# Kernel optimization log

Hardware: AMD Instinct MI355X
Metric: run time of the kernel (lower is better)

Reference implementation:

```python
import jax, jax.numpy as jnp
import numpy as np

K = 10
BN_EPS = 1e-5


def _edgeconv(x, W, b, gamma, beta):
    """DGCNN EdgeConv: kNN on x, edge feat [x_i, x_j - x_i], Linear->(BN)->ReLU, max over k.
    x: [N, C]; W: [2C, Cout]; gamma/beta: [Cout] or None."""
    sq = jnp.sum(x * x, axis=1)                      # [N]
    dist = sq[:, None] + sq[None, :] - 2.0 * (x @ x.T)  # [N, N] squared dists
    _, idx = jax.lax.top_k(-dist, K)                 # [N, K] (includes self)
    xj = x[idx]                                      # [N, K, C] gather
    xi = jnp.broadcast_to(x[:, None, :], xj.shape)   # [N, K, C]
    e = jnp.concatenate([xi, xj - xi], axis=-1)      # [N, K, 2C]
    h = e @ W + b                                    # [N, K, Cout]
    if gamma is not None:                            # BatchNorm1d (training-mode batch stats)
        mu = h.mean(axis=(0, 1))
        var = h.var(axis=(0, 1))
        h = (h - mu) * jax.lax.rsqrt(var + BN_EPS) * gamma + beta
    h = jax.nn.relu(h)
    return h.max(axis=1)                             # [N, Cout]


def _aggregate(f, seg_ids, num_segments):
    return jax.ops.segment_max(f, seg_ids, num_segments=num_segments)


def setup_inputs() -> dict:
    key = jax.random.key(0)
    ks = jax.random.split(key, 12)
    N, B = 16384, 64
    x = jax.random.normal(ks[0], (N, 3), dtype=jnp.float32)
    n_pts = jnp.full((B,), N // B, dtype=jnp.int32)

    def lin(k, fi, fo):
        s = 1.0 / np.sqrt(fi)
        kw, kb = jax.random.split(k)
        return (jax.random.uniform(kw, (fi, fo), jnp.float32, -s, s),
                jax.random.uniform(kb, (fo,), jnp.float32, -s, s))

    W1, b1 = lin(ks[1], 6, 64)
    W2, b2 = lin(ks[2], 128, 64)
    W3, b3 = lin(ks[3], 128, 64)
    W4, b4 = lin(ks[4], 128, 64)
    Wp, bp = lin(ks[5], 256, 128)
    g1 = jnp.ones((64,), jnp.float32); be1 = jnp.zeros((64,), jnp.float32)
    g3 = jnp.ones((64,), jnp.float32); be3 = jnp.zeros((64,), jnp.float32)
    return {"x": x, "n_pts": n_pts,
            "W1": W1, "b1": b1, "g1": g1, "be1": be1,
            "W2": W2, "b2": b2,
            "W3": W3, "b3": b3, "g3": g3, "be3": be3,
            "W4": W4, "b4": b4,
            "Wp": Wp, "bp": bp}


def reference(x, n_pts, W1, b1, g1, be1, W2, b2, W3, b3, g3, be3, W4, b4, Wp, bp):
    N = x.shape[0]
    B = n_pts.shape[0]
    seg_ids = jnp.repeat(jnp.arange(B, dtype=jnp.int32), n_pts, total_repeat_length=N)

    f1 = _edgeconv(x,  W1, b1, g1,  be1)   # [N, 64]
    f2 = _edgeconv(f1, W2, b2, None, None)
    f3 = _edgeconv(f2, W3, b3, g3,  be3)
    f4 = _edgeconv(f3, W4, b4, None, None)

    p = jnp.concatenate([_aggregate(f, seg_ids, B) for f in (f1, f2, f3, f4)], axis=1)  # [B, 256]
    f = jnp.tanh(p @ Wp + bp)              # [B, 128]
    f = f / (jnp.linalg.norm(f, axis=1, keepdims=True) + 1e-9)
    return f
```

## Files before the change

kernel.cpp:

```cpp
#include <hip/hip_runtime.h>
#include <hip/hip_bf16.h>

constexpr int N = 16384;
constexpr int KNN = 10;
constexpr int CF = 64;
constexpr int NS64 = 12;
constexpr int NS3 = 6;

#define FBIG 1e30f

typedef __attribute__((ext_vector_type(8))) __bf16 bfv8;
typedef __attribute__((ext_vector_type(4))) float f32x4;

#define TOPK_INSERT(dval, jval)                                            \
  if ((dval) < bmax) {                                                     \
    float mv = bd[0]; int slot = 0;                                        \
    _Pragma("unroll") for (int s_ = 1; s_ < 10; ++s_)                      \
      if (bd[s_] > mv) { mv = bd[s_]; slot = s_; }                         \
    _Pragma("unroll") for (int s_ = 0; s_ < 10; ++s_)                      \
      if (slot == s_) { bd[s_] = (dval); bi[s_] = (jval); }                \
    bmax = bd[0];                                                          \
    _Pragma("unroll") for (int s_ = 1; s_ < 10; ++s_)                      \
      bmax = fmaxf(bmax, bd[s_]);                                          \
  }

__device__ inline ushort bf16_rne(float x) {
  unsigned u = __float_as_uint(x);
  return (ushort)((u + 0x7FFFu + ((u >> 16) & 1u)) >> 16);
}
__device__ inline float bf16_to_f(ushort h) { return __uint_as_float(((unsigned)h) << 16); }

__global__ __launch_bounds__(256) void pack3_kernel(const float* __restrict__ X,
                                                    float4* __restrict__ xp) {
  int i = blockIdx.x * 256 + threadIdx.x;
  float x0 = X[3 * i], x1 = X[3 * i + 1], x2 = X[3 * i + 2];
  float s = fmaf(x0, x0, fmaf(x1, x1, x2 * x2));
  xp[i] = make_float4(x0, x1, x2, s);
}

__global__ __launch_bounds__(256) void prep128s_kernel(const float* __restrict__ X,
                                                       ushort* __restrict__ Xp,
                                                       float* __restrict__ sq) {
  int i = blockIdx.x * 256 + threadIdx.x;
  int n = i >> 4, k4 = (i & 15) << 2;
  float4 v = ((const float4*)X)[i];
  float vv[4] = {v.x, v.y, v.z, v.w};
  ushort h[4], lo[4];
#pragma unroll
  for (int k = 0; k < 4; ++k) {
    h[k] = bf16_rne(vv[k]);
    lo[k] = bf16_rne(vv[k] - bf16_to_f(h[k]));
  }
  ushort* row = Xp + (size_t)n * 128;
  *(ushort4*)(row + k4) = make_ushort4(h[0], h[1], h[2], h[3]);
  *(ushort4*)(row + 64 + k4) = make_ushort4(lo[0], lo[1], lo[2], lo[3]);
  float ps = fmaf(vv[0], vv[0], fmaf(vv[1], vv[1], fmaf(vv[2], vv[2], vv[3] * vv[3])));
#pragma unroll
  for (int m = 1; m < 16; m <<= 1) ps += __shfl_xor(ps, m, 16);
  if ((threadIdx.x & 15) == 0) sq[n] = ps;
}


__global__ __launch_bounds__(256, 3) void knn64w_kernel(const ushort* __restrict__ Xp,
                                                        const float* __restrict__ sq,
                                                        int* __restrict__ gtauI,
                                                        float* __restrict__ dpart,
                                                        ushort* __restrict__ ipart) {
  __shared__ float bufD[4][64 * 17];
  __shared__ ushort bufI[4][64 * 18];
  __shared__ __align__(16) float tauS[4][64];
  __shared__ int cntS[4][64];

  const int tid = threadIdx.x;
  const int w = tid >> 6, l = tid & 63, lp = l & 15, g = l >> 4;
  const int rg = blockIdx.x / NS64, cs = blockIdx.x % NS64;
  const int wbase = rg * 256 + w * 64;
  const int myrow = wbase + l;
  const int c0 = (1024 * cs) / NS64, c1 = (1024 * (cs + 1)) / NS64;

  tauS[w][l] = FBIG;
  cntS[w][l] = 0;
  __builtin_amdgcn_wave_barrier();

  bfv8 aH1[4], aH2[4], aL1[4], aL2[4];
#pragma unroll
  for (int rt = 0; rt < 4; ++rt) {
    const size_t ao = (size_t)(wbase + rt * 16 + lp) * 128 + g * 8;
    aH1[rt] = *(const bfv8*)&Xp[ao];
    aH2[rt] = *(const bfv8*)&Xp[ao + 32];
    aL1[rt] = *(const bfv8*)&Xp[ao + 64];
    aL2[rt] = *(const bfv8*)&Xp[ao + 96];
  }
  float sqi[16];
#pragma unroll
  for (int rt = 0; rt < 4; ++rt)
#pragma unroll
    for (int r = 0; r < 4; ++r) sqi[rt * 4 + r] = sq[wbase + rt * 16 + g * 4 + r];

  float bd[10]; int bi[10]; float bmax = FBIG; float lastPub = FBIG;
#pragma unroll
  for (int s = 0; s < 10; ++s) { bd[s] = FBIG; bi[s] = 0x7fffffff; }
  int gt = 0x7F7F7F7F;

  for (int t = c0; t < c1; ++t) {
    const int bcol = t * 16 + lp;
    const size_t bo = (size_t)bcol * 128 + g * 8;
    bfv8 bc0 = *(const bfv8*)&Xp[bo];
    bfv8 bc1 = *(const bfv8*)&Xp[bo + 32];
    bfv8 bc2 = *(const bfv8*)&Xp[bo + 64];
    bfv8 bc3 = *(const bfv8*)&Xp[bo + 96];
    float sjc = sq[bcol];
    int gtn = gtauI[myrow];

    __builtin_amdgcn_wave_barrier();
    {
      const int c = cntS[w][l];
      if (c) {
        const float* bD = &bufD[w][l * 17];
        const ushort* bI = &bufI[w][l * 18];
#pragma unroll 1
        for (int j = 0; j < c; ++j) {
          float d = bD[j];
          int ii = (int)bI[j];
          TOPK_INSERT(d, ii);
        }
        cntS[w][l] = 0;
      }
      tauS[w][l] = fminf(bmax, __int_as_float(gt));
      if (bmax < lastPub) {
        atomicMin(&gtauI[myrow], __float_as_int(bmax));
        lastPub = bmax;
      }
    }
    __builtin_amdgcn_wave_barrier();
    gt = gtn;

#pragma unroll
    for (int rt = 0; rt < 4; ++rt) {
      f32x4 acc = {0.f, 0.f, 0.f, 0.f};
      acc = __builtin_amdgcn_mfma_f32_16x16x32_bf16(aH1[rt], bc0, acc, 0, 0, 0);
      acc = __builtin_amdgcn_mfma_f32_16x16x32_bf16(aH2[rt], bc1, acc, 0, 0, 0);
      acc = __builtin_amdgcn_mfma_f32_16x16x32_bf16(aH1[rt], bc2, acc, 0, 0, 0);
      acc = __builtin_amdgcn_mfma_f32_16x16x32_bf16(aH2[rt], bc3, acc, 0, 0, 0);
      acc = __builtin_amdgcn_mfma_f32_16x16x32_bf16(aL1[rt], bc0, acc, 0, 0, 0);
      acc = __builtin_amdgcn_mfma_f32_16x16x32_bf16(aL2[rt], bc1, acc, 0, 0, 0);
      f32x4 taur = *(const f32x4*)&tauS[w][rt * 16 + g * 4];
#pragma unroll
      for (int r = 0; r < 4; ++r) {
        float d = fmaf(-2.f, acc[r], sqi[rt * 4 + r] + sjc);
        if (d < taur[r]) {
          int rloc = rt * 16 + g * 4 + r;
          int pos = atomicAdd(&cntS[w][rloc], 1);
          bufD[w][rloc * 17 + pos] = d;
          bufI[w][rloc * 18 + pos] = (ushort)bcol;
        }
      }
    }
  }

  __builtin_amdgcn_wave_barrier();
  {
    const int c = cntS[w][l];
    const float* bD = &bufD[w][l * 17];
    const ushort* bI = &bufI[w][l * 18];
#pragma unroll 1
    for (int j = 0; j < c; ++j) {
      float d = bD[j];
      int ii = (int)bI[j];
      TOPK_INSERT(d, ii);
    }
  }
  float* dp = dpart + ((size_t)cs * N + myrow) * 10;
  ushort* ip = ipart + ((size_t)cs * N + myrow) * 10;
#pragma unroll
  for (int s = 0; s < 10; ++s) { dp[s] = bd[s]; ip[s] = (ushort)bi[s]; }
}

__global__ __launch_bounds__(256, 3) void knn3w_kernel(const float4* __restrict__ xp,
                                                       float* __restrict__ dpart,
                                                       ushort* __restrict__ ipart) {
  __shared__ float bufD[4][32 * 17];
  __shared__ ushort bufI[4][32 * 18];
  __shared__ __align__(16) float tauS[4][32];
  __shared__ int cntS[4][32];

  const int tid = threadIdx.x;
  const int w = tid >> 6, l = tid & 63, lp = l & 15, g = l >> 4;
  const int rg = blockIdx.x / NS3, cs = blockIdx.x % NS3;
  const int wbase = rg * 128 + w * 32;
  const int c0 = (1024 * cs) / NS3, c1 = (1024 * (cs + 1)) / NS3;

  if (l < 32) { tauS[w][l] = FBIG; cntS[w][l] = 0; }
  __builtin_amdgcn_wave_barrier();

  float4 rw[8];
#pragma unroll
  for (int rt = 0; rt < 2; ++rt)
#pragma unroll
    for (int r = 0; r < 4; ++r) rw[rt * 4 + r] = xp[wbase + rt * 16 + g * 4 + r];

  float bd[10]; int bi[10]; float bmax = FBIG;
#pragma unroll
  for (int s = 0; s < 10; ++s) { bd[s] = FBIG; bi[s] = 0x7fffffff; }

  float4 oc = xp[c0 * 16 + lp];
  for (int t = c0; t < c1; ++t) {
    float4 on;
    if (t + 1 < c1) on = xp[(t + 1) * 16 + lp];
    __builtin_amdgcn_wave_barrier();
    if (l < 32) {
      const int c = cntS[w][l];
      if (c) {
        const float* bD = &bufD[w][l * 17];
        const ushort* bI = &bufI[w][l * 18];
#pragma unroll 1
        for (int j = 0; j < c; ++j) {
          float d = bD[j];
          int ii = (int)bI[j];
          TOPK_INSERT(d, ii);
        }
        cntS[w][l] = 0;
        tauS[w][l] = bmax;
      }
    }
    __builtin_amdgcn_wave_barrier();
    const int lcol = t * 16 + lp;
#pragma unroll
    for (int rt = 0; rt < 2; ++rt) {
      f32x4 taur = *(const f32x4*)&tauS[w][rt * 16 + g * 4];
#pragma unroll
      for (int r = 0; r < 4; ++r) {
        const float4 m = rw[rt * 4 + r];
        float dot = fmaf(m.x, oc.x, fmaf(m.y, oc.y, m.z * oc.z));
        float d = fmaf(-2.f, dot, m.w + oc.w);
        if (d < taur[r]) {
          int rloc = rt * 16 + g * 4 + r;
          int pos = atomicAdd(&cntS[w][rloc], 1);
          bufD[w][rloc * 17 + pos] = d;
          bufI[w][rloc * 18 + pos] = (ushort)lcol;
        }
      }
    }
    oc = on;
  }
  __builtin_amdgcn_wave_barrier();
  if (l < 32) {
    const int c = cntS[w][l];
    const float* bD = &bufD[w][l * 17];
    const ushort* bI = &bufI[w][l * 18];
#pragma unroll 1
    for (int j = 0; j < c; ++j) {
      float d = bD[j];
      int ii = (int)bI[j];
      TOPK_INSERT(d, ii);
    }
    const int row = wbase + l;
    float* dp = dpart + ((size_t)cs * N + row) * 10;
    ushort* ip = ipart + ((size_t)cs * N + row) * 10;
#pragma unroll
    for (int s = 0; s < 10; ++s) { dp[s] = bd[s]; ip[s] = (ushort)bi[s]; }
  }
}

template <int S>
__global__ __launch_bounds__(256) void merge_kernel(const float* __restrict__ dpart,
                                                    const ushort* __restrict__ ipart,
                                                    ushort* __restrict__ idx_out) {
  const int row = blockIdx.x * 256 + threadIdx.x;
  float d[S * 10]; int id_[S * 10];
#pragma unroll
  for (int p = 0; p < S; ++p)
#pragma unroll
    for (int s = 0; s < 10; ++s) {
      d[p * 10 + s] = dpart[((size_t)p * N + row) * 10 + s];
      id_[p * 10 + s] = (int)ipart[((size_t)p * N + row) * 10 + s];
    }
#pragma unroll
  for (int t = 0; t < 10; ++t) {
    float dm = d[0]; int im = id_[0]; int slot = 0;
#pragma unroll
    for (int e = 1; e < S * 10; ++e) {
      bool better = (d[e] < dm) || (d[e] == dm && id_[e] < im);
      if (better) { dm = d[e]; im = id_[e]; slot = e; }
    }
    idx_out[(size_t)row * 10 + t] = (ushort)im;
#pragma unroll
    for (int e = 0; e < S * 10; ++e)
      if (e == slot) d[e] = FBIG;
  }
}

__global__ __launch_bounds__(256) void uv_kernel(const float* __restrict__ Xf, int CIN,
                                                 const float* __restrict__ W,
                                                 const float* __restrict__ bias,
                                                 float* __restrict__ U, float* __restrict__ V) {
  int tid = threadIdx.x;
  int c = tid & 63, p = tid >> 6;
  int n = blockIdx.x * 4 + p;
  const float* xr = Xf + (size_t)n * CIN;
  float vt = 0.f, vb = 0.f;
  for (int m = 0; m < CIN; ++m) {
    float xm = xr[m];
    vt = fmaf(xm, W[m * 64 + c], vt);
    vb = fmaf(xm, W[(CIN + m) * 64 + c], vb);
  }
  U[(size_t)n * 64 + c] = vb;
  V[(size_t)n * 64 + c] = vt - vb + bias[c];
}

__global__ __launch_bounds__(256) void stats_kernel(const float* __restrict__ U,
                                                    const float* __restrict__ V,
                                                    const ushort* __restrict__ idx,
                                                    float* __restrict__ accum) {
  int tid = threadIdx.x;
  int c = tid & 63, p = tid >> 6;
  int base = blockIdx.x * 64;
  float s = 0.f, s2 = 0.f;
  for (int ch = 0; ch < 16; ++ch) {
    int n = base + ch * 4 + p;
    float vn = V[(size_t)n * 64 + c];
    const ushort* in_ = idx + (size_t)n * 10;
#pragma unroll
    for (int k = 0; k < 10; ++k) {
      float h = vn + U[(size_t)in_[k] * 64 + c];
      s += h;
      s2 = fmaf(h, h, s2);
    }
  }
  __shared__ float red[256], red2[256];
  red[tid] = s; red2[tid] = s2;
  __syncthreads();
  if (tid < 64) {
    float ts = red[tid] + red[64 + tid] + red[128 + tid] + red[192 + tid];
    float t2 = red2[tid] + red2[64 + tid] + red2[128 + tid] + red2[192 + tid];
    atomicAdd(&accum[tid], ts);
    atomicAdd(&accum[64 + tid], t2);
  }
}

__global__ void bnfin_kernel(const float* __restrict__ accum,
                             const float* __restrict__ gamma,
                             const float* __restrict__ beta,
                             float* __restrict__ scale, float* __restrict__ shift) {
  int c = threadIdx.x;
  float inv = 1.f / (float)(N * KNN);
  float mu = accum[c] * inv;
  float var = accum[64 + c] * inv - mu * mu;
  float sc = gamma[c] * rsqrtf(var + 1e-5f);
  scale[c] = sc;
  shift[c] = fmaf(-mu, sc, beta[c]);
}

__global__ __launch_bounds__(256) void apply_kernel(const float* __restrict__ U,
                                                    const float* __restrict__ V,
                                                    const ushort* __restrict__ idx,
                                                    const float* __restrict__ scale,
                                                    const float* __restrict__ shift,
                                                    int use_bn, float* __restrict__ Fout) {
  int tid = threadIdx.x;
  int c = tid & 63, p = tid >> 6;
  int n = blockIdx.x * 4 + p;
  float sc = use_bn ? scale[c] : 1.f;
  float sh = use_bn ? shift[c] : 0.f;
  float vn = V[(size_t)n * 64 + c];
  const ushort* in_ = idx + (size_t)n * 10;
  float m = 0.f;
#pragma unroll
  for (int k = 0; k < 10; ++k) {
    float h = vn + U[(size_t)in_[k] * 64 + c];
    m = fmaxf(m, fmaf(h, sc, sh));
  }
  Fout[(size_t)n * 64 + c] = m;
}

__global__ __launch_bounds__(256) void pool1_kernel(const float* __restrict__ f1,
                                                    const float* __restrict__ f2,
                                                    const float* __restrict__ f3,
                                                    const float* __restrict__ f4,
                                                    const int* __restrict__ n_pts,
                                                    float* __restrict__ Pp) {
  int b = blockIdx.x >> 2;
  int q = blockIdx.x & 3;
  int c = threadIdx.x;
  int off = 0;
  for (int i = 0; i < b; ++i) off += n_pts[i];
  int cnt_ = n_pts[b];
  int s0 = off + (cnt_ * q) / 4;
  int s1 = off + (cnt_ * (q + 1)) / 4;
  const float* f = (c < 64) ? f1 : (c < 128) ? f2 : (c < 192) ? f3 : f4;
  int ch = c & 63;
  float m = -3.4e38f;
  for (int t = s0; t < s1; ++t) m = fmaxf(m, f[(size_t)t * 64 + ch]);
  Pp[((size_t)q * 64 + b) * 256 + c] = m;
}

__global__ __launch_bounds__(256) void pool2_kernel(const float* __restrict__ Pp,
                                                    float* __restrict__ P) {
  int b = blockIdx.x;
  int c = threadIdx.x;
  float m = Pp[(size_t)b * 256 + c];
#pragma unroll
  for (int q = 1; q < 4; ++q) m = fmaxf(m, Pp[((size_t)q * 64 + b) * 256 + c]);
  P[b * 256 + c] = m;
}

__global__ __launch_bounds__(128) void head_kernel(const float* __restrict__ P,
                                                   const float* __restrict__ Wp,
                                                   const float* __restrict__ bp,
                                                   float* __restrict__ out) {
  int b = blockIdx.x;
  int c = threadIdx.x;
  __shared__ float ps[256];
  ps[c] = P[b * 256 + c];
  ps[128 + c] = P[b * 256 + 128 + c];
  __syncthreads();
  float acc = bp[c];
  for (int m = 0; m < 256; ++m) acc = fmaf(ps[m], Wp[m * 128 + c], acc);
  float t = tanhf(acc);
  __shared__ float red[128];
  red[c] = t * t;
  __syncthreads();
  for (int s = 64; s > 0; s >>= 1) {
    if (c < s) red[c] += red[c + s];
    __syncthreads();
  }
  float nrm = sqrtf(red[0]);
  out[b * 128 + c] = t / (nrm + 1e-9f);
}

extern "C" void kernel_launch(void* const* d_in, const int* in_sizes, int n_in,
                              void* d_out, int out_size, void* d_ws, size_t ws_size,
                              hipStream_t stream) {
  const float* x = (const float*)d_in[0];
  const int* n_pts = (const int*)d_in[1];
  const float* W1 = (const float*)d_in[2];
  const float* b1 = (const float*)d_in[3];
  const float* g1 = (const float*)d_in[4];
  const float* be1 = (const float*)d_in[5];
  const float* W2 = (const float*)d_in[6];
  const float* b2 = (const float*)d_in[7];
  const float* W3 = (const float*)d_in[8];
  const float* b3 = (const float*)d_in[9];
  const float* g3 = (const float*)d_in[10];
  const float* be3 = (const float*)d_in[11];
  const float* W4 = (const float*)d_in[12];
  const float* b4 = (const float*)d_in[13];
  const float* Wp = (const float*)d_in[14];
  const float* bp = (const float*)d_in[15];
  float* out = (float*)d_out;

  char* w = (char*)d_ws;
  auto alloc = [&](size_t bytes) {
    char* p = w;
    w += (bytes + 255) & ~(size_t)255;
    return p;
  };
  const size_t FS = (size_t)N * 64 * 4;
  float* f1 = (float*)alloc(FS);
  float* f2 = (float*)alloc(FS);
  float* f3 = (float*)alloc(FS);
  float* f4 = (float*)alloc(FS);
  float* Ub = (float*)alloc(FS);
  float* dpartf = (float*)alloc((size_t)NS64 * N * 10 * 4);
  ushort* iparti = (ushort*)alloc((size_t)NS64 * N * 10 * 2);
  float4* xp = (float4*)alloc((size_t)N * 16);
  float* sqb = (float*)alloc((size_t)N * 4);
  int* gtauI = (int*)alloc((size_t)N * 4);
  ushort* idxb = (ushort*)alloc((size_t)N * 10 * 2);
  float* accum = (float*)alloc(512);
  float* scaleb = (float*)alloc(256);
  float* shiftb = (float*)alloc(256);
  float* Pb = (float*)alloc((size_t)64 * 256 * 4);
  float* Ppart = (float*)alloc((size_t)4 * 64 * 256 * 4);
  ushort* Xp128 = (ushort*)Ub;
  float* Vb = dpartf;
  (void)ws_size; (void)n_in; (void)in_sizes; (void)out_size;

  auto run_layer = [&](const float* fin, int cin, const float* W, const float* b,
                       const float* g, const float* be, int use_bn, float* fout) {
    if (cin == 3) {
      pack3_kernel<<<N / 256, 256, 0, stream>>>(fin, xp);
      knn3w_kernel<<<128 * NS3, 256, 0, stream>>>(xp, dpartf, iparti);
      merge_kernel<NS3><<<N / 256, 256, 0, stream>>>(dpartf, iparti, idxb);
    } else {
      hipMemsetAsync(gtauI, 0x7F, (size_t)N * 4, stream);
      prep128s_kernel<<<N * 64 / 4 / 256, 256, 0, stream>>>(fin, Xp128, sqb);
      knn64w_kernel<<<64 * NS64, 256, 0, stream>>>(Xp128, sqb, gtauI, dpartf, iparti);
      merge_kernel<NS64><<<N / 256, 256, 0, stream>>>(dpartf, iparti, idxb);
    }
    uv_kernel<<<N / 4, 256, 0, stream>>>(fin, cin, W, b, Ub, Vb);
    if (use_bn) {
      hipMemsetAsync(accum, 0, 512, stream);
      stats_kernel<<<256, 256, 0, stream>>>(Ub, Vb, idxb, accum);
      bnfin_kernel<<<1, 64, 0, stream>>>(accum, g, be, scaleb, shiftb);
    }
    apply_kernel<<<N / 4, 256, 0, stream>>>(Ub, Vb, idxb, scaleb, shiftb, use_bn, fout);
  };

  run_layer(x, 3, W1, b1, g1, be1, 1, f1);
  run_layer(f1, 64, W2, b2, nullptr, nullptr, 0, f2);
  run_layer(f2, 64, W3, b3, g3, be3, 1, f3);
  run_layer(f3, 64, W4, b4, nullptr, nullptr, 0, f4);
  pool1_kernel<<<256, 256, 0, stream>>>(f1, f2, f3, f4, n_pts, Ppart);
  pool2_kernel<<<64, 256, 0, stream>>>(Ppart, Pb);
  head_kernel<<<64, 128, 0, stream>>>(Pb, Wp, bp, out);
}
```

Before: 1.371 ms.

## Share kNN thresholds globally in 3-D layer and fold memsets and pool2 into kernels

The 3-D kNN kernel is restructured so that each wave covers 64 rows, and the column space is split into 12 slices instead of 6. Each row publishes its current top-k bound through a global atomicMin, so the other column-slice blocks can prune candidates earlier. The hipMemsetAsync calls for the threshold and BN accumulator buffers move into the pack and prep kernels, and the pool2 reduction is fused into the head kernel, which removes launches. In exchange, the change adds global atomics and per-iteration global loads in the kNN loop and raises register pressure from 16 row vectors per thread.

```diff
diff --git a/kernel.cpp b/kernel.cpp
--- a/kernel.cpp
+++ b/kernel.cpp
@@ -5,7 +5,7 @@
 constexpr int KNN = 10;
 constexpr int CF = 64;
 constexpr int NS64 = 12;
-constexpr int NS3 = 6;
+constexpr int NS3 = 12;
 
 #define FBIG 1e30f
 
@@ -31,16 +31,22 @@
 __device__ inline float bf16_to_f(ushort h) { return __uint_as_float(((unsigned)h) << 16); }
 
 __global__ __launch_bounds__(256) void pack3_kernel(const float* __restrict__ X,
-                                                    float4* __restrict__ xp) {
+                                                    float4* __restrict__ xp,
+                                                    int* __restrict__ gtauI,
+                                                    float* __restrict__ accum) {
   int i = blockIdx.x * 256 + threadIdx.x;
   float x0 = X[3 * i], x1 = X[3 * i + 1], x2 = X[3 * i + 2];
   float s = fmaf(x0, x0, fmaf(x1, x1, x2 * x2));
   xp[i] = make_float4(x0, x1, x2, s);
+  gtauI[i] = 0x7F7F7F7F;
+  if (blockIdx.x == 0 && threadIdx.x < 128) accum[threadIdx.x] = 0.f;
 }
 
 __global__ __launch_bounds__(256) void prep128s_kernel(const float* __restrict__ X,
                                                        ushort* __restrict__ Xp,
-                                                       float* __restrict__ sq) {
+                                                       float* __restrict__ sq,
+                                                       int* __restrict__ gtauI,
+                                                       float* __restrict__ accum) {
   int i = blockIdx.x * 256 + threadIdx.x;
   int n = i >> 4, k4 = (i & 15) << 2;
   float4 v = ((const float4*)X)[i];
@@ -57,7 +63,11 @@
   float ps = fmaf(vv[0], vv[0], fmaf(vv[1], vv[1], fmaf(vv[2], vv[2], vv[3] * vv[3])));
 #pragma unroll
   for (int m = 1; m < 16; m <<= 1) ps += __shfl_xor(ps, m, 16);
-  if ((threadIdx.x & 15) == 0) sq[n] = ps;
+  if ((threadIdx.x & 15) == 0) {
+    sq[n] = ps;
+    gtauI[n] = 0x7F7F7F7F;
+  }
+  if (blockIdx.x == 0 && threadIdx.x < 128) accum[threadIdx.x] = 0.f;
 }
 
 
@@ -176,39 +186,44 @@
   for (int s = 0; s < 10; ++s) { dp[s] = bd[s]; ip[s] = (ushort)bi[s]; }
 }
 
-__global__ __launch_bounds__(256, 3) void knn3w_kernel(const float4* __restrict__ xp,
+__global__ __launch_bounds__(256, 3) void knn3g_kernel(const float4* __restrict__ xp,
+                                                       int* __restrict__ gtauI,
                                                        float* __restrict__ dpart,
                                                        ushort* __restrict__ ipart) {
-  __shared__ float bufD[4][32 * 17];
-  __shared__ ushort bufI[4][32 * 18];
-  __shared__ __align__(16) float tauS[4][32];
-  __shared__ int cntS[4][32];
+  __shared__ float bufD[4][64 * 17];
+  __shared__ ushort bufI[4][64 * 18];
+  __shared__ __align__(16) float tauS[4][64];
+  __shared__ int cntS[4][64];
 
   const int tid = threadIdx.x;
   const int w = tid >> 6, l = tid & 63, lp = l & 15, g = l >> 4;
   const int rg = blockIdx.x / NS3, cs = blockIdx.x % NS3;
-  const int wbase = rg * 128 + w * 32;
+  const int wbase = rg * 256 + w * 64;
+  const int myrow = wbase + l;
   const int c0 = (1024 * cs) / NS3, c1 = (1024 * (cs + 1)) / NS3;
 
-  if (l < 32) { tauS[w][l] = FBIG; cntS[w][l] = 0; }
+  tauS[w][l] = FBIG;
+  cntS[w][l] = 0;
   __builtin_amdgcn_wave_barrier();
 
-  float4 rw[8];
-#pragma unroll
-  for (int rt = 0; rt < 2; ++rt)
+  float4 rw[16];
+#pragma unroll
+  for (int rt = 0; rt < 4; ++rt)
 #pragma unroll
     for (int r = 0; r < 4; ++r) rw[rt * 4 + r] = xp[wbase + rt * 16 + g * 4 + r];
 
-  float bd[10]; int bi[10]; float bmax = FBIG;
+  float bd[10]; int bi[10]; float bmax = FBIG; float lastPub = FBIG;
 #pragma unroll
   for (int s = 0; s < 10; ++s) { bd[s] = FBIG; bi[s] = 0x7fffffff; }
-
-  float4 oc = xp[c0 * 16 + lp];
+  int gt = 0x7F7F7F7F;
+
   for (int t = c0; t < c1; ++t) {
-    float4 on;
-    if (t + 1 < c1) on = xp[(t + 1) * 16 + lp];
+    const int bcol = t * 16 + lp;
+    const float4 oc = xp[bcol];
+    int gtn = gtauI[myrow];
+
     __builtin_amdgcn_wave_barrier();
-    if (l < 32) {
+    {
       const int c = cntS[w][l];
       if (c) {
         const float* bD = &bufD[w][l * 17];
@@ -220,13 +235,18 @@
           TOPK_INSERT(d, ii);
         }
         cntS[w][l] = 0;
-        tauS[w][l] = bmax;
       }
+      tauS[w][l] = fminf(bmax, __int_as_float(gt));
+      if (bmax < lastPub) {
+        atomicMin(&gtauI[myrow], __float_as_int(bmax));
+        lastPub = bmax;
+      }
     }
     __builtin_amdgcn_wave_barrier();
-    const int lcol = t * 16 + lp;
-#pragma unroll
-    for (int rt = 0; rt < 2; ++rt) {
+    gt = gtn;
+
+#pragma unroll
+    for (int rt = 0; rt < 4; ++rt) {
       f32x4 taur = *(const f32x4*)&tauS[w][rt * 16 + g * 4];
 #pragma unroll
       for (int r = 0; r < 4; ++r) {
@@ -237,14 +257,14 @@
           int rloc = rt * 16 + g * 4 + r;
           int pos = atomicAdd(&cntS[w][rloc], 1);
           bufD[w][rloc * 17 + pos] = d;
-          bufI[w][rloc * 18 + pos] = (ushort)lcol;
+          bufI[w][rloc * 18 + pos] = (ushort)bcol;
         }
       }
     }
-    oc = on;
-  }
+  }
+
   __builtin_amdgcn_wave_barrier();
-  if (l < 32) {
+  {
     const int c = cntS[w][l];
     const float* bD = &bufD[w][l * 17];
     const ushort* bI = &bufI[w][l * 18];
@@ -254,12 +274,11 @@
       int ii = (int)bI[j];
       TOPK_INSERT(d, ii);
     }
-    const int row = wbase + l;
-    float* dp = dpart + ((size_t)cs * N + row) * 10;
-    ushort* ip = ipart + ((size_t)cs * N + row) * 10;
-#pragma unroll
-    for (int s = 0; s < 10; ++s) { dp[s] = bd[s]; ip[s] = (ushort)bi[s]; }
-  }
+  }
+  float* dp = dpart + ((size_t)cs * N + myrow) * 10;
+  ushort* ip = ipart + ((size_t)cs * N + myrow) * 10;
+#pragma unroll
+  for (int s = 0; s < 10; ++s) { dp[s] = bd[s]; ip[s] = (ushort)bi[s]; }
 }
 
 template <int S>
@@ -394,25 +413,21 @@
   Pp[((size_t)q * 64 + b) * 256 + c] = m;
 }
 
-__global__ __launch_bounds__(256) void pool2_kernel(const float* __restrict__ Pp,
-                                                    float* __restrict__ P) {
-  int b = blockIdx.x;
-  int c = threadIdx.x;
-  float m = Pp[(size_t)b * 256 + c];
-#pragma unroll
-  for (int q = 1; q < 4; ++q) m = fmaxf(m, Pp[((size_t)q * 64 + b) * 256 + c]);
-  P[b * 256 + c] = m;
-}
-
-__global__ __launch_bounds__(128) void head_kernel(const float* __restrict__ P,
+__global__ __launch_bounds__(128) void head_kernel(const float* __restrict__ Pp,
                                                    const float* __restrict__ Wp,
                                                    const float* __restrict__ bp,
                                                    float* __restrict__ out) {
   int b = blockIdx.x;
   int c = threadIdx.x;
   __shared__ float ps[256];
-  ps[c] = P[b * 256 + c];
-  ps[128 + c] = P[b * 256 + 128 + c];
+#pragma unroll
+  for (int j = 0; j < 2; ++j) {
+    int cc = c + j * 128;
+    float m = Pp[(size_t)b * 256 + cc];
+#pragma unroll
+    for (int q = 1; q < 4; ++q) m = fmaxf(m, Pp[((size_t)q * 64 + b) * 256 + cc]);
+    ps[cc] = m;
+  }
   __syncthreads();
   float acc = bp[c];
   for (int m = 0; m < 256; ++m) acc = fmaf(ps[m], Wp[m * 128 + c], acc);
@@ -470,7 +485,6 @@
   float* accum = (float*)alloc(512);
   float* scaleb = (float*)alloc(256);
   float* shiftb = (float*)alloc(256);
-  float* Pb = (float*)alloc((size_t)64 * 256 * 4);
   float* Ppart = (float*)alloc((size_t)4 * 64 * 256 * 4);
   ushort* Xp128 = (ushort*)Ub;
   float* Vb = dpartf;
@@ -479,18 +493,16 @@
   auto run_layer = [&](const float* fin, int cin, const float* W, const float* b,
                        const float* g, const float* be, int use_bn, float* fout) {
     if (cin == 3) {
-      pack3_kernel<<<N / 256, 256, 0, stream>>>(fin, xp);
-      knn3w_kernel<<<128 * NS3, 256, 0, stream>>>(xp, dpartf, iparti);
+      pack3_kernel<<<N / 256, 256, 0, stream>>>(fin, xp, gtauI, accum);
+      knn3g_kernel<<<64 * NS3, 256, 0, stream>>>(xp, gtauI, dpartf, iparti);
       merge_kernel<NS3><<<N / 256, 256, 0, stream>>>(dpartf, iparti, idxb);
     } else {
-      hipMemsetAsync(gtauI, 0x7F, (size_t)N * 4, stream);
-      prep128s_kernel<<<N * 64 / 4 / 256, 256, 0, stream>>>(fin, Xp128, sqb);
+      prep128s_kernel<<<N * 64 / 4 / 256, 256, 0, stream>>>(fin, Xp128, sqb, gtauI, accum);
       knn64w_kernel<<<64 * NS64, 256, 0, stream>>>(Xp128, sqb, gtauI, dpartf, iparti);
       merge_kernel<NS64><<<N / 256, 256, 0, stream>>>(dpartf, iparti, idxb);
     }
     uv_kernel<<<N / 4, 256, 0, stream>>>(fin, cin, W, b, Ub, Vb);
     if (use_bn) {
-      hipMemsetAsync(accum, 0, 512, stream);
       stats_kernel<<<256, 256, 0, stream>>>(Ub, Vb, idxb, accum);
       bnfin_kernel<<<1, 64, 0, stream>>>(accum, g, be, scaleb, shiftb);
     }
@@ -502,6 +514,5 @@
   run_layer(f2, 64, W3, b3, g3, be3, 1, f3);
   run_layer(f3, 64, W4, b4, nullptr, nullptr, 0, f4);
   pool1_kernel<<<256, 256, 0, stream>>>(f1, f2, f3, f4, n_pts, Ppart);
-  pool2_kernel<<<64, 256, 0, stream>>>(Ppart, Pb);
-  head_kernel<<<64, 128, 0, stream>>>(Pb, Wp, bp, out);
-}
+  head_kernel<<<64, 128, 0, stream>>>(Ppart, Wp, bp, out);
+}
```

Result: no change. 1.355 ms (-1.2%).
